# Performance work log

Hardware: AMD Instinct MI355X
Metric: run time of the kernel (lower is better)

## Reference

```python
import jax, jax.numpy as jnp
import numpy as np

TEMPERATURE = 0.1

def _l2norm(x):
    return x / jnp.linalg.norm(x, axis=-1, keepdims=True)

def setup_inputs() -> dict:
    key = jax.random.key(0)
    k1, k2, k3 = jax.random.split(key, 3)
    N_AUG, B, F, Q = 2, 256, 128, 65536
    V = _l2norm(jax.random.normal(k1, (N_AUG, B, F), dtype=jnp.float32))
    L = _l2norm(jax.random.normal(k2, (B, F), dtype=jnp.float32))
    queue = _l2norm(jax.random.normal(k3, (Q, F), dtype=jnp.float32))
    return {"V": V, "L": L, "queue": queue}

def reference(V, L, queue):
    # V: (J, B, F), L: (B, F), queue: (Q, F)
    J, B, F = V.shape
    inv_t = 1.0 / TEMPERATURE
    # pos[j, b] = V[j, b] . L[b] / T  (diagonal batch pairings)
    pos = jnp.einsum('jbf,bf->jb', V, L) * inv_t                 # (J, B)
    # qlog[j, b, q] = V[j, b] . queue[q] / T
    qlog = jnp.einsum('jbf,qf->jbq', V, queue) * inv_t           # (J, B, Q)
    # Original: denom[j,b] = log( sum_i exp(pos[j,i]) + sum_q exp(qlog[j,b,q]) )
    # == logsumexp over the concatenation of pos[j,:] and qlog[j,b,:].
    bat = jnp.broadcast_to(pos[:, None, :], (J, B, B))           # (J, B, B)
    combined = jnp.concatenate([bat, qlog], axis=-1)             # (J, B, B+Q)
    denom = jax.nn.logsumexp(combined, axis=-1)                  # (J, B)
    # loss = -(1/B) * sum_{b} sum_{j} (pos[j,b] - denom[j,b])
    loss = -jnp.sum(pos - denom) / B
    return loss
```

## Files before the change

### kernel.cpp

```cpp
#include <hip/hip_runtime.h>


typedef float  float4v __attribute__((ext_vector_type(4)));
typedef short  short8  __attribute__((ext_vector_type(8)));

__device__ __forceinline__ unsigned short f2bf(float f) {
    union { float f; unsigned u; } v; v.f = f;
    unsigned r = v.u + 0x7FFFu + ((v.u >> 16) & 1u);
    return (unsigned short)(r >> 16);
}


__global__ __launch_bounds__(256) void prep2_kernel(
        const float* __restrict__ V, const float* __restrict__ L,
        unsigned short* __restrict__ abf, float* __restrict__ pos) {
    const int tid = threadIdx.x;
    if (blockIdx.x < 64) {
        const int gt = blockIdx.x * 256 + tid;
        const float4 v = ((const float4*)V)[gt];
        uint2 p;
        p.x = (unsigned)f2bf(v.x) | ((unsigned)f2bf(v.y) << 16);
        p.y = (unsigned)f2bf(v.z) | ((unsigned)f2bf(v.w) << 16);
        ((uint2*)abf)[gt] = p;
    } else {
        const int blk  = blockIdx.x - 64;
        const int w    = tid >> 6;
        const int lane = tid & 63;
        #pragma unroll
        for (int i = 0; i < 2; ++i) {
            const int r = blk * 8 + w * 2 + i;
            const int b = r & 255;
            const float2 v = *reinterpret_cast<const float2*>(V + r * 128 + lane * 2);
            const float2 l = *reinterpret_cast<const float2*>(L + b * 128 + lane * 2);
            float p = v.x * l.x + v.y * l.y;
            #pragma unroll
            for (int off = 32; off; off >>= 1) p += __shfl_xor(p, off);
            if (lane == 0) pos[r] = 10.0f * p;
        }
    }
}

__global__ __launch_bounds__(256, 2) void gemm_exp_fused_kernel(
        const unsigned short* __restrict__ abf,
        const float* __restrict__ Qf,
        float* __restrict__ gbuf) {
    __shared__ unsigned short Bs[128 * 128];
    __shared__ float rowsum[256];

    const int tid  = threadIdx.x;
    const int bid  = blockIdx.x;
    const int nb   = bid * 128;

    const int w    = tid >> 6;
    const int lane = tid & 63;
    const int quad = lane >> 4;
    const int l16  = lane & 15;
    const int wrow = w * 64;

    #pragma unroll
    for (int i = 0; i < 16; ++i) {
        const int idx = i * 256 + tid;
        const int row = idx >> 5;
        const int c4  = idx & 31;
        const float4 q = *reinterpret_cast<const float4*>(Qf + (nb + row) * 128 + c4 * 4);
        uint2 p;
        p.x = (unsigned)f2bf(q.x) | ((unsigned)f2bf(q.y) << 16);
        p.y = (unsigned)f2bf(q.z) | ((unsigned)f2bf(q.w) << 16);
        const int chunk = (c4 >> 1) ^ (row & 15);
        *reinterpret_cast<uint2*>(&Bs[row * 128 + (chunk << 3) + ((c4 & 1) << 2)]) = p;
    }
    __syncthreads();

    #pragma unroll 1
    for (int mt = 0; mt < 2; ++mt) {
        const int m0 = mt * 256;

        short8 a[4][4];
        #pragma unroll
        for (int mi = 0; mi < 4; ++mi)
            #pragma unroll
            for (int kk = 0; kk < 4; ++kk)
                a[mi][kk] = *(const short8*)&abf[(m0 + wrow + mi * 16 + l16) * 128
                                                 + (kk * 4 + quad) * 8];

        float rs[4][4];
        #pragma unroll
        for (int mi = 0; mi < 4; ++mi)
            #pragma unroll
            for (int r = 0; r < 4; ++r) rs[mi][r] = 0.0f;

        #pragma unroll
        for (int sub = 0; sub < 2; ++sub) {
            float4v acc[4][4];
            #pragma unroll
            for (int mi = 0; mi < 4; ++mi)
                #pragma unroll
                for (int ni = 0; ni < 4; ++ni)
                    acc[mi][ni] = (float4v){0.f, 0.f, 0.f, 0.f};

            #pragma unroll
            for (int kk = 0; kk < 4; ++kk) {
                const int c = kk * 4 + quad;
                short8 b[4];
                #pragma unroll
                for (int ni = 0; ni < 4; ++ni) {
                    const int row = sub * 64 + ni * 16 + l16;
                    b[ni] = *(const short8*)&Bs[row * 128 + ((c ^ (row & 15)) << 3)];
                }
                #pragma unroll
                for (int mi = 0; mi < 4; ++mi)
                    #pragma unroll
                    for (int ni = 0; ni < 4; ++ni)
                        acc[mi][ni] = __builtin_amdgcn_mfma_f32_16x16x32_bf16(
                            a[mi][kk], b[ni], acc[mi][ni], 0, 0, 0);
            }

            #pragma unroll
            for (int mi = 0; mi < 4; ++mi)
                #pragma unroll
                for (int ni = 0; ni < 4; ++ni)
                    #pragma unroll
                    for (int r = 0; r < 4; ++r)
                        rs[mi][r] += exp2f(acc[mi][ni][r] * 14.426950408889634f);
        }

        #pragma unroll
        for (int mi = 0; mi < 4; ++mi)
            #pragma unroll
            for (int r = 0; r < 4; ++r) {
                float v = rs[mi][r];
                v += __shfl_xor(v, 1);
                v += __shfl_xor(v, 2);
                v += __shfl_xor(v, 4);
                v += __shfl_xor(v, 8);
                if (l16 == 0) rowsum[wrow + mi * 16 + quad * 4 + r] = v;
            }
        __syncthreads();
        gbuf[bid * 512 + mt * 256 + tid] = rowsum[tid];
        __syncthreads();
    }
}

__global__ __launch_bounds__(256) void reduce_k_kernel(
        const float* __restrict__ gbuf, float* __restrict__ gbuf2) {
    const int g = blockIdx.x * 256 + threadIdx.x;
    const int m = g & 511;
    const int s = g >> 9;
    float acc = 0.0f;
    #pragma unroll
    for (int k = 0; k < 16; ++k)
        acc += gbuf[(s * 16 + k) * 512 + m];
    gbuf2[s * 512 + m] = acc;
}

__global__ __launch_bounds__(1024) void finalize_fused_kernel(
        const float* __restrict__ pos,
        const float* __restrict__ gbuf2,
        float* __restrict__ out) {
    __shared__ float wsum[16];
    __shared__ float Sp[2];
    const int tid  = threadIdx.x;
    const int w    = tid >> 6;
    const int lane = tid & 63;

    float e = (tid < 512) ? __expf(pos[tid]) : 0.0f;
    #pragma unroll
    for (int off = 32; off; off >>= 1) e += __shfl_xor(e, off);
    if (lane == 0) wsum[w] = e;
    __syncthreads();
    if (tid == 0) {
        Sp[0] = wsum[0] + wsum[1] + wsum[2] + wsum[3];
        Sp[1] = wsum[4] + wsum[5] + wsum[6] + wsum[7];
    }
    __syncthreads();

    const int m = tid >> 1;
    const int h = tid & 1;
    float s = 0.0f;
    #pragma unroll
    for (int k = 0; k < 16; ++k)
        s += gbuf2[(h * 16 + k) * 512 + m];
    s += __shfl_xor(s, 1);

    float contrib = 0.0f;
    if (h == 0) contrib = pos[m] - __logf(Sp[m >> 8] + s);
    #pragma unroll
    for (int off = 32; off; off >>= 1) contrib += __shfl_xor(contrib, off);
    __syncthreads();
    if (lane == 0) wsum[w] = contrib;
    __syncthreads();
    if (tid == 0) {
        float tot = 0.0f;
        #pragma unroll
        for (int i = 0; i < 16; ++i) tot += wsum[i];
        out[0] = -tot / 256.0f;
    }
}


__global__ void prep_kernel(const float* __restrict__ V,
                            const float* __restrict__ L,
                            float* __restrict__ pos,
                            float* __restrict__ Sq) {
    const int blk  = blockIdx.x;
    const int tid  = threadIdx.x;
    if (tid < 8) Sq[blk * 8 + tid] = 0.0f;
    const int w    = tid >> 6;
    const int lane = tid & 63;
    #pragma unroll
    for (int i = 0; i < 2; ++i) {
        const int r = blk * 8 + w * 2 + i;
        const int b = r & 255;
        const float2 v = *reinterpret_cast<const float2*>(V + r * 128 + lane * 2);
        const float2 l = *reinterpret_cast<const float2*>(L + b * 128 + lane * 2);
        float p = v.x * l.x + v.y * l.y;
        #pragma unroll
        for (int off = 32; off; off >>= 1) p += __shfl_xor(p, off);
        if (lane == 0) pos[r] = 10.0f * p;
    }
}

__global__ __launch_bounds__(256) void gemm_exp_fallback(
        const float* __restrict__ V,
        const float* __restrict__ Q,
        float* __restrict__ Sq) {
    __shared__ unsigned short As[128 * 128];
    __shared__ unsigned short Bs[128 * 128];
    const int tid = threadIdx.x;
    const int m0  = blockIdx.y * 128;
    const int n0  = blockIdx.x * 128;
    #pragma unroll
    for (int i = 0; i < 16; ++i) {
        const int idx = i * 256 + tid;
        const int row = idx >> 5;
        const int c4  = idx & 31;
        const float4 a = *reinterpret_cast<const float4*>(V + (m0 + row) * 128 + c4 * 4);
        const float4 b = *reinterpret_cast<const float4*>(Q + (n0 + row) * 128 + c4 * 4);
        const int chunk = ((c4 >> 1) ^ (row & 15));
        const int off   = row * 128 + (chunk << 3) + ((c4 & 1) << 2);
        const uint2 pa = make_uint2((unsigned)f2bf(a.x) | ((unsigned)f2bf(a.y) << 16),
                                    (unsigned)f2bf(a.z) | ((unsigned)f2bf(a.w) << 16));
        const uint2 pb = make_uint2((unsigned)f2bf(b.x) | ((unsigned)f2bf(b.y) << 16),
                                    (unsigned)f2bf(b.z) | ((unsigned)f2bf(b.w) << 16));
        *reinterpret_cast<uint2*>(&As[off]) = pa;
        *reinterpret_cast<uint2*>(&Bs[off]) = pb;
    }
    __syncthreads();
    const int w    = tid >> 6;
    const int lane = tid & 63;
    const int quad = lane >> 4;
    const int l16  = lane & 15;
    const int wrow = (w >> 1) * 64;
    const int wcol = (w & 1) * 64;
    float4v acc[4][4];
    #pragma unroll
    for (int mi = 0; mi < 4; ++mi)
        #pragma unroll
        for (int ni = 0; ni < 4; ++ni)
            acc[mi][ni] = (float4v){0.f, 0.f, 0.f, 0.f};
    #pragma unroll
    for (int kk = 0; kk < 4; ++kk) {
        const int kchunk = kk * 4 + quad;
        short8 a[4], b[4];
        #pragma unroll
        for (int mi = 0; mi < 4; ++mi) {
            const int row = wrow + mi * 16 + l16;
            a[mi] = *reinterpret_cast<const short8*>(&As[row * 128 + ((kchunk ^ (row & 15)) << 3)]);
        }
        #pragma unroll
        for (int ni = 0; ni < 4; ++ni) {
            const int row = wcol + ni * 16 + l16;
            b[ni] = *reinterpret_cast<const short8*>(&Bs[row * 128 + ((kchunk ^ (row & 15)) << 3)]);
        }
        #pragma unroll
        for (int mi = 0; mi < 4; ++mi)
            #pragma unroll
            for (int ni = 0; ni < 4; ++ni)
                acc[mi][ni] = __builtin_amdgcn_mfma_f32_16x16x32_bf16(a[mi], b[ni], acc[mi][ni], 0, 0, 0);
    }
    __syncthreads();
    float* rowsum = reinterpret_cast<float*>(As);
    #pragma unroll
    for (int mi = 0; mi < 4; ++mi) {
        float rsv[4] = {0.f, 0.f, 0.f, 0.f};
        #pragma unroll
        for (int ni = 0; ni < 4; ++ni)
            #pragma unroll
            for (int r = 0; r < 4; ++r)
                rsv[r] += __expf(10.0f * acc[mi][ni][r]);
        #pragma unroll
        for (int r = 0; r < 4; ++r) {
            float vsum = rsv[r];
            vsum += __shfl_xor(vsum, 1);
            vsum += __shfl_xor(vsum, 2);
            vsum += __shfl_xor(vsum, 4);
            vsum += __shfl_xor(vsum, 8);
            if (l16 == 0)
                rowsum[(w & 1) * 128 + wrow + mi * 16 + quad * 4 + r] = vsum;
        }
    }
    __syncthreads();
    if (tid < 128)
        atomicAdd(&Sq[m0 + tid], rowsum[tid] + rowsum[128 + tid]);
}

__global__ void finalize_kernel(const float* __restrict__ pos,
                                const float* __restrict__ Sq,
                                float* __restrict__ out) {
    __shared__ float wsum[8];
    __shared__ float Sp[2];
    const int tid  = threadIdx.x;
    const int w    = tid >> 6;
    const int lane = tid & 63;
    const float p = pos[tid];
    float e = __expf(p);
    #pragma unroll
    for (int off = 32; off; off >>= 1) e += __shfl_xor(e, off);
    if (lane == 0) wsum[w] = e;
    __syncthreads();
    if (tid == 0) {
        Sp[0] = wsum[0] + wsum[1] + wsum[2] + wsum[3];
        Sp[1] = wsum[4] + wsum[5] + wsum[6] + wsum[7];
    }
    __syncthreads();
    const int j = tid >> 8;
    float contrib = p - __logf(Sp[j] + Sq[tid]);
    #pragma unroll
    for (int off = 32; off; off >>= 1) contrib += __shfl_xor(contrib, off);
    if (lane == 0) wsum[w] = contrib;
    __syncthreads();
    if (tid == 0) {
        float tot = 0.f;
        #pragma unroll
        for (int i = 0; i < 8; ++i) tot += wsum[i];
        out[0] = -tot / 256.0f;
    }
}


extern "C" void kernel_launch(void* const* d_in, const int* in_sizes, int n_in,
                              void* d_out, int out_size, void* d_ws, size_t ws_size,
                              hipStream_t stream) {
    const float* V     = (const float*)d_in[0];
    const float* L     = (const float*)d_in[1];
    const float* queue = (const float*)d_in[2];
    float* out = (float*)d_out;

    const size_t need = (size_t)512 * 128 * 2 + 512 * 4
                      + (size_t)512 * 512 * 4 + (size_t)32 * 512 * 4;
    if (ws_size >= need) {
        unsigned short* abf = (unsigned short*)d_ws;
        float* pos   = (float*)(abf + 512 * 128);
        float* gbuf  = pos + 512;
        float* gbuf2 = gbuf + (size_t)512 * 512;
        prep2_kernel<<<128, 256, 0, stream>>>(V, L, abf, pos);
        gemm_exp_fused_kernel<<<512, 256, 0, stream>>>(abf, queue, gbuf);
        reduce_k_kernel<<<64, 256, 0, stream>>>(gbuf, gbuf2);
        finalize_fused_kernel<<<1, 1024, 0, stream>>>(pos, gbuf2, out);
    } else {
        float* pos = (float*)d_ws;
        float* Sq  = pos + 512;
        prep_kernel<<<64, 256, 0, stream>>>(V, L, pos, Sq);
        dim3 grid(512, 4);
        gemm_exp_fallback<<<grid, 256, 0, stream>>>(V, queue, Sq);
        finalize_kernel<<<1, 512, 0, stream>>>(pos, Sq, out);
    }
}
```

Measured before the change: 102.8 us.

## Fuse reduction and finalize into GEMM kernel via atomics and last-block ticket

The separate reduce and finalize kernels and the positive-logit computation in prep are removed. Each GEMM block now atomically adds its row sums into a 512-entry Sq buffer, and the last block to finish (found with an atomic ticket) computes the positive logits, their exp sums and the final loss. This cuts the launch count from four to two and drops the 1 MB partial-sum buffer round trip. In exchange it adds atomic contention on Sq (512 blocks x 512 adds), makes the float summation order nondeterministic, and leaves a serial tail in the last block.

```diff
diff --git a/kernel.cpp b/kernel.cpp
--- a/kernel.cpp
+++ b/kernel.cpp
@@ -11,41 +11,33 @@
 }
 
 
-__global__ __launch_bounds__(256) void prep2_kernel(
-        const float* __restrict__ V, const float* __restrict__ L,
-        unsigned short* __restrict__ abf, float* __restrict__ pos) {
+__global__ __launch_bounds__(256) void prep_fast_kernel(
+        const float* __restrict__ V, unsigned short* __restrict__ abf,
+        float* __restrict__ Sq, unsigned int* __restrict__ ticket) {
     const int tid = threadIdx.x;
-    if (blockIdx.x < 64) {
-        const int gt = blockIdx.x * 256 + tid;
-        const float4 v = ((const float4*)V)[gt];
-        uint2 p;
-        p.x = (unsigned)f2bf(v.x) | ((unsigned)f2bf(v.y) << 16);
-        p.y = (unsigned)f2bf(v.z) | ((unsigned)f2bf(v.w) << 16);
-        ((uint2*)abf)[gt] = p;
-    } else {
-        const int blk  = blockIdx.x - 64;
-        const int w    = tid >> 6;
-        const int lane = tid & 63;
-        #pragma unroll
-        for (int i = 0; i < 2; ++i) {
-            const int r = blk * 8 + w * 2 + i;
-            const int b = r & 255;
-            const float2 v = *reinterpret_cast<const float2*>(V + r * 128 + lane * 2);
-            const float2 l = *reinterpret_cast<const float2*>(L + b * 128 + lane * 2);
-            float p = v.x * l.x + v.y * l.y;
-            #pragma unroll
-            for (int off = 32; off; off >>= 1) p += __shfl_xor(p, off);
-            if (lane == 0) pos[r] = 10.0f * p;
-        }
-    }
-}
-
-__global__ __launch_bounds__(256, 2) void gemm_exp_fused_kernel(
+    const int gt  = blockIdx.x * 256 + tid;
+    const float4 v = ((const float4*)V)[gt];
+    uint2 p;
+    p.x = (unsigned)f2bf(v.x) | ((unsigned)f2bf(v.y) << 16);
+    p.y = (unsigned)f2bf(v.z) | ((unsigned)f2bf(v.w) << 16);
+    ((uint2*)abf)[gt] = p;
+    if (blockIdx.x == 0) {
+        Sq[tid] = 0.0f;
+        Sq[tid + 256] = 0.0f;
+        if (tid == 0) *ticket = 0u;
+    }
+}
+
+__global__ __launch_bounds__(256, 2) void mega_kernel(
         const unsigned short* __restrict__ abf,
         const float* __restrict__ Qf,
-        float* __restrict__ gbuf) {
+        const float* __restrict__ V, const float* __restrict__ L,
+        float* __restrict__ Sq, unsigned int* __restrict__ ticket,
+        float* __restrict__ out) {
     __shared__ unsigned short Bs[128 * 128];
     __shared__ float rowsum[256];
+    __shared__ float red[2][4];
+    __shared__ unsigned int lastFlag;
 
     const int tid  = threadIdx.x;
     const int bid  = blockIdx.x;
@@ -136,65 +128,54 @@
                 if (l16 == 0) rowsum[wrow + mi * 16 + quad * 4 + r] = v;
             }
         __syncthreads();
-        gbuf[bid * 512 + mt * 256 + tid] = rowsum[tid];
+        atomicAdd(&Sq[m0 + tid], rowsum[tid]);
         __syncthreads();
     }
-}
-
-__global__ __launch_bounds__(256) void reduce_k_kernel(
-        const float* __restrict__ gbuf, float* __restrict__ gbuf2) {
-    const int g = blockIdx.x * 256 + threadIdx.x;
-    const int m = g & 511;
-    const int s = g >> 9;
-    float acc = 0.0f;
-    #pragma unroll
-    for (int k = 0; k < 16; ++k)
-        acc += gbuf[(s * 16 + k) * 512 + m];
-    gbuf2[s * 512 + m] = acc;
-}
-
-__global__ __launch_bounds__(1024) void finalize_fused_kernel(
-        const float* __restrict__ pos,
-        const float* __restrict__ gbuf2,
-        float* __restrict__ out) {
-    __shared__ float wsum[16];
-    __shared__ float Sp[2];
-    const int tid  = threadIdx.x;
-    const int w    = tid >> 6;
-    const int lane = tid & 63;
-
-    float e = (tid < 512) ? __expf(pos[tid]) : 0.0f;
-    #pragma unroll
-    for (int off = 32; off; off >>= 1) e += __shfl_xor(e, off);
-    if (lane == 0) wsum[w] = e;
-    __syncthreads();
-    if (tid == 0) {
-        Sp[0] = wsum[0] + wsum[1] + wsum[2] + wsum[3];
-        Sp[1] = wsum[4] + wsum[5] + wsum[6] + wsum[7];
-    }
-    __syncthreads();
-
-    const int m = tid >> 1;
-    const int h = tid & 1;
-    float s = 0.0f;
-    #pragma unroll
-    for (int k = 0; k < 16; ++k)
-        s += gbuf2[(h * 16 + k) * 512 + m];
-    s += __shfl_xor(s, 1);
-
-    float contrib = 0.0f;
-    if (h == 0) contrib = pos[m] - __logf(Sp[m >> 8] + s);
+
+    __threadfence();
+    __syncthreads();
+    if (tid == 0) lastFlag = (atomicAdd(ticket, 1u) == 511u) ? 1u : 0u;
+    __syncthreads();
+    if (lastFlag == 0u) return;
+    __threadfence();
+
+    float p01[2];
+    #pragma unroll
+    for (int h = 0; h < 2; ++h) {
+        const float4* vr = (const float4*)(V + (h * 256 + tid) * 128);
+        const float4* lr = (const float4*)(L + tid * 128);
+        float d = 0.0f;
+        #pragma unroll
+        for (int i = 0; i < 32; ++i) {
+            const float4 a4 = vr[i];
+            const float4 b4 = lr[i];
+            d += a4.x * b4.x + a4.y * b4.y + a4.z * b4.z + a4.w * b4.w;
+        }
+        p01[h] = 10.0f * d;
+    }
+
+    #pragma unroll
+    for (int h = 0; h < 2; ++h) {
+        float e = __expf(p01[h]);
+        #pragma unroll
+        for (int off = 32; off; off >>= 1) e += __shfl_xor(e, off);
+        if (lane == 0) red[h][w] = e;
+    }
+    __syncthreads();
+    const float Sp0 = red[0][0] + red[0][1] + red[0][2] + red[0][3];
+    const float Sp1 = red[1][0] + red[1][1] + red[1][2] + red[1][3];
+
+    const float s0 = atomicAdd(&Sq[tid], 0.0f);
+    const float s1 = atomicAdd(&Sq[256 + tid], 0.0f);
+
+    float contrib = (p01[0] - __logf(Sp0 + s0)) + (p01[1] - __logf(Sp1 + s1));
     #pragma unroll
     for (int off = 32; off; off >>= 1) contrib += __shfl_xor(contrib, off);
     __syncthreads();
-    if (lane == 0) wsum[w] = contrib;
-    __syncthreads();
-    if (tid == 0) {
-        float tot = 0.0f;
-        #pragma unroll
-        for (int i = 0; i < 16; ++i) tot += wsum[i];
-        out[0] = -tot / 256.0f;
-    }
+    if (lane == 0) red[0][w] = contrib;
+    __syncthreads();
+    if (tid == 0)
+        out[0] = -(red[0][0] + red[0][1] + red[0][2] + red[0][3]) / 256.0f;
 }
 
 
@@ -346,17 +327,13 @@
     const float* queue = (const float*)d_in[2];
     float* out = (float*)d_out;
 
-    const size_t need = (size_t)512 * 128 * 2 + 512 * 4
-                      + (size_t)512 * 512 * 4 + (size_t)32 * 512 * 4;
+    const size_t need = (size_t)512 * 128 * 2 + 512 * 4 + 64;
     if (ws_size >= need) {
         unsigned short* abf = (unsigned short*)d_ws;
-        float* pos   = (float*)(abf + 512 * 128);
-        float* gbuf  = pos + 512;
-        float* gbuf2 = gbuf + (size_t)512 * 512;
-        prep2_kernel<<<128, 256, 0, stream>>>(V, L, abf, pos);
-        gemm_exp_fused_kernel<<<512, 256, 0, stream>>>(abf, queue, gbuf);
-        reduce_k_kernel<<<64, 256, 0, stream>>>(gbuf, gbuf2);
-        finalize_fused_kernel<<<1, 1024, 0, stream>>>(pos, gbuf2, out);
+        float* Sq           = (float*)(abf + 512 * 128);
+        unsigned int* tick  = (unsigned int*)(Sq + 512);
+        prep_fast_kernel<<<64, 256, 0, stream>>>(V, abf, Sq, tick);
+        mega_kernel<<<512, 256, 0, stream>>>(abf, queue, V, L, Sq, tick, out);
     } else {
         float* pos = (float*)d_ws;
         float* Sq  = pos + 512;
```

After: 151.6 us. 1.48x slower.
